# Performance work log

Measured on AMD Instinct MI355X. Metric: run time of the kernel, lower is better.

## Reference

```python
import jax, jax.numpy as jnp
import numpy as np
from jax import lax

ALIVE_THRESHOLD = 0.1
GROWTH_BOOST = 1.0  # forward default arg

_SX = jnp.array([[-1., 0., 1.], [-2., 0., 2.], [-1., 0., 1.]], dtype=jnp.float32)
_SY = jnp.array([[-1., -2., -1.], [0., 0., 0.], [1., 2., 1.]], dtype=jnp.float32)


def _depthwise3x3(x, k):
    # x: [B,C,H,W], k: [3,3] -> depthwise conv, padding 1 (SAME)
    C = x.shape[1]
    w = jnp.tile(k[None, None], (C, 1, 1, 1))  # [C,1,3,3]
    return lax.conv_general_dilated(
        x, w, window_strides=(1, 1), padding='SAME',
        dimension_numbers=('NCHW', 'OIHW', 'NCHW'), feature_group_count=C)


def _avg_pool3x3(x):
    # torch avg_pool2d(k=3, stride=1, pad=1, count_include_pad=True) == sum window / 9 with zero pad
    w = jnp.ones((1, 1, 3, 3), dtype=x.dtype) / 9.0
    return lax.conv_general_dilated(
        x, w, window_strides=(1, 1), padding='SAME',
        dimension_numbers=('NCHW', 'OIHW', 'NCHW'))


def setup_inputs() -> dict:
    key = jax.random.key(0)
    ks = jax.random.split(key, 5)
    B, C, H, W = 16, 8, 512, 512
    x = jax.random.normal(ks[0], (B, C, H, W), dtype=jnp.float32)
    # kaiming_normal_(a=0.3) -> std = sqrt(2/(1+a^2)) / sqrt(fan_in)
    gain = float(np.sqrt(2.0 / (1.0 + 0.3 ** 2)))
    w1 = jax.random.normal(ks[1], (32, 24), dtype=jnp.float32) * (gain / np.sqrt(24))
    w2 = jax.random.normal(ks[2], (32, 32), dtype=jnp.float32) * (gain / np.sqrt(32))
    w3 = jax.random.normal(ks[3], (8, 32), dtype=jnp.float32) * (gain / np.sqrt(32))
    b1 = jnp.full((32,), 0.05, dtype=jnp.float32)
    b2 = jnp.full((32,), 0.05, dtype=jnp.float32)
    b3 = jnp.full((8,), 0.05, dtype=jnp.float32)
    growth_rate = jnp.array([0.3], dtype=jnp.float32)
    return {'x': x, 'w1': w1, 'b1': b1, 'w2': w2, 'b2': b2,
            'w3': w3, 'b3': b3, 'growth_rate': growth_rate}


def reference(x, w1, b1, w2, b2, w3, b3, growth_rate):
    # perceive: [x, sobel_x(x), sobel_y(x)] -> [B, 3C, H, W]
    perceived = jnp.concatenate([x, _depthwise3x3(x, _SX), _depthwise3x3(x, _SY)], axis=1)
    # per-pixel MLP (1x1 convs)
    h = jax.nn.relu(jnp.einsum('bchw,oc->bohw', perceived, w1) + b1[None, :, None, None])
    h = jax.nn.relu(jnp.einsum('bchw,oc->bohw', h, w2) + b2[None, :, None, None])
    dx = jnp.einsum('bchw,oc->bohw', h, w3) + b3[None, :, None, None]
    dx = dx * growth_rate[0] * GROWTH_BOOST
    # alive masking / growth zones
    alive_mask = (x[:, 3:4] > ALIVE_THRESHOLD).astype(x.dtype)
    alive_ratio = jnp.mean(alive_mask)
    neighbor_alive = _avg_pool3x3(alive_mask)
    growth_zones = (neighbor_alive > 0.01).astype(x.dtype) * 0.2  # [B,1,H,W]
    boost = jnp.where(alive_ratio < 0.2, growth_zones, jnp.zeros_like(growth_zones))
    dx = jnp.concatenate([dx[:, :3], dx[:, 3:4] + boost, dx[:, 4:]], axis=1)
    new_x = jnp.clip(x + dx, -1.0, 1.0)
    alpha = jnp.clip(new_x[:, 3:4], 0.0, 1.0)
    return jnp.concatenate([new_x[:, :3], alpha, new_x[:, 4:]], axis=1)
```

## Files before the change

### kernel.cpp

```cpp
#include <hip/hip_runtime.h>

namespace {

typedef __attribute__((ext_vector_type(8))) short short8;
typedef __attribute__((ext_vector_type(4))) float f32x4;
typedef __attribute__((ext_vector_type(4))) unsigned int uint4v;

constexpr int kH = 512, kW = 512, kB = 16, kC = 8;
constexpr int kHW = kH * kW;
constexpr int kBS = kC * kHW;
constexpr int TW = 64, TH = 4;
constexpr int TWP = TW + 2, THP = TH + 2;

__global__ __launch_bounds__(256)
void alive_count_kernel(const float* __restrict__ x, int* __restrict__ cnt) {
    __shared__ int sdata[4];
    const int tid = threadIdx.x;
    const int total4 = kB * kHW / 4;
    int idx = blockIdx.x * 256 + tid;
    const int stride = gridDim.x * 256;
    int local = 0;
    const float4* x4 = (const float4*)x;
    for (int i = idx; i < total4; i += stride) {
        int b = i >> 16;
        int off = i & 65535;
        float4 v = x4[(size_t)b * (kBS / 4) + (3 * kHW / 4) + off];
        local += (v.x > 0.1f) + (v.y > 0.1f) + (v.z > 0.1f) + (v.w > 0.1f);
    }
    for (int off = 32; off > 0; off >>= 1)
        local += __shfl_down(local, off, 64);
    if ((tid & 63) == 0) sdata[tid >> 6] = local;
    __syncthreads();
    if (tid == 0) atomicAdd(cnt, sdata[0] + sdata[1] + sdata[2] + sdata[3]);
}

__device__ inline unsigned int cvt_pk_bf16(float a, float b) {
    unsigned int r;
    asm("v_cvt_pk_bf16_f32 %0, %1, %2" : "=v"(r) : "v"(a), "v"(b));
    return r;
}
__device__ inline void split_pair(float a, float b, unsigned int& h, unsigned int& l) {
    h = cvt_pk_bf16(a, b);
    float ra = a - __builtin_bit_cast(float, h << 16);
    float rb = b - __builtin_bit_cast(float, h & 0xffff0000u);
    l = cvt_pk_bf16(ra, rb);
}
__device__ inline short8 frag_of(unsigned int u0, unsigned int u1,
                                 unsigned int u2, unsigned int u3) {
    uint4v u = {u0, u1, u2, u3};
    return __builtin_bit_cast(short8, u);
}
__device__ inline void split_frag(f32x4 a, f32x4 b, short8& hi, short8& lo) {
    unsigned int h0, h1, h2, h3, l0, l1, l2, l3;
    split_pair(a.x, a.y, h0, l0);
    split_pair(a.z, a.w, h1, l1);
    split_pair(b.x, b.y, h2, l2);
    split_pair(b.z, b.w, h3, l3);
    hi = frag_of(h0, h1, h2, h3);
    lo = frag_of(l0, l1, l2, l3);
}
__device__ inline f32x4 mfma4(short8 wh, short8 wl, short8 bh, short8 bl, f32x4 acc) {
    acc = __builtin_amdgcn_mfma_f32_16x16x32_bf16(wh, bh, acc, 0, 0, 0);
    acc = __builtin_amdgcn_mfma_f32_16x16x32_bf16(wh, bl, acc, 0, 0, 0);
    acc = __builtin_amdgcn_mfma_f32_16x16x32_bf16(wl, bh, acc, 0, 0, 0);
    acc = __builtin_amdgcn_mfma_f32_16x16x32_bf16(wl, bl, acc, 0, 0, 0);
    return acc;
}
__device__ inline f32x4 relu4(f32x4 v) {
    v.x = fmaxf(v.x, 0.f); v.y = fmaxf(v.y, 0.f);
    v.z = fmaxf(v.z, 0.f); v.w = fmaxf(v.w, 0.f);
    return v;
}
__device__ inline void transpose_to_bfrag(f32x4 v0, f32x4 v1, int i1, int i2,
                                          bool oddq, bool lowq,
                                          short8& bh, short8& bl) {
    unsigned int Ah, Al, Bh, Bl, Ch, Cl, Dh, Dl;
    split_pair(v0.x, v0.y, Ah, Al);
    split_pair(v0.z, v0.w, Bh, Bl);
    split_pair(v1.x, v1.y, Ch, Cl);
    split_pair(v1.z, v1.w, Dh, Dl);
    int f1h = __builtin_amdgcn_ds_bpermute(i1, (int)(oddq ? Ch : Ah));
    int f2h = __builtin_amdgcn_ds_bpermute(i2, (int)(oddq ? Ah : Ch));
    int f3h = __builtin_amdgcn_ds_bpermute(i1, (int)(oddq ? Dh : Bh));
    int f4h = __builtin_amdgcn_ds_bpermute(i2, (int)(oddq ? Bh : Dh));
    int f1l = __builtin_amdgcn_ds_bpermute(i1, (int)(oddq ? Cl : Al));
    int f2l = __builtin_amdgcn_ds_bpermute(i2, (int)(oddq ? Al : Cl));
    int f3l = __builtin_amdgcn_ds_bpermute(i1, (int)(oddq ? Dl : Bl));
    int f4l = __builtin_amdgcn_ds_bpermute(i2, (int)(oddq ? Bl : Dl));
    bh = frag_of(lowq ? (unsigned)f1h : (unsigned)f2h, lowq ? (unsigned)f3h : (unsigned)f4h,
                 lowq ? (unsigned)f2h : (unsigned)f1h, lowq ? (unsigned)f4h : (unsigned)f3h);
    bl = frag_of(lowq ? (unsigned)f1l : (unsigned)f2l, lowq ? (unsigned)f3l : (unsigned)f4l,
                 lowq ? (unsigned)f2l : (unsigned)f1l, lowq ? (unsigned)f4l : (unsigned)f3l);
}

__global__ __launch_bounds__(256)
void nca_fused_kernel(const float* __restrict__ x,
                      const float* __restrict__ w1, const float* __restrict__ b1,
                      const float* __restrict__ w2, const float* __restrict__ b2,
                      const float* __restrict__ w3, const float* __restrict__ b3,
                      const float* __restrict__ growth,
                      const int* __restrict__ alive_cnt,
                      float* __restrict__ out) {
    __shared__ float tile[kC][THP][TWP];
    __shared__ __align__(16) unsigned int s_hi[4][64][20];
    __shared__ __align__(16) unsigned int s_lo[4][64][20];
    __shared__ __align__(16) float s_d[4][64][8];

    const int w0 = blockIdx.x * TW;
    const int h0 = blockIdx.y * TH;
    const int b  = blockIdx.z;
    const int tid = threadIdx.x;
    const int lane = tid & 63;
    const int wv = tid >> 6;
    const int m = lane & 15;
    const int q = lane >> 4;
    const bool oddq = (q & 1) != 0;
    const bool lowq = q < 2;
    const int brq = ((q & 1) << 1) | (q >> 1);
    const int i1 = (m + 16 * brq) << 2;
    const int i2 = (m + 16 * (brq ^ 1)) << 2;
    const float* xb = x + b * kBS;

    f32x4 zero4 = {0.f, 0.f, 0.f, 0.f};
    short8 w1h[2], w1l[2], w2h[2], w2l[2], w3h, w3l;
    f32x4 bias1[2], bias2[2], bias3;
#pragma unroll
    for (int mo = 0; mo < 2; ++mo) {
        int o = mo * 16 + m;
        int off = (q < 3) ? (o * 24 + q * 8) : 0;
        f32x4 wa = *(const f32x4*)(w1 + off);
        f32x4 wb = *(const f32x4*)(w1 + off + 4);
        if (q == 3) { wa = zero4; wb = zero4; }
        split_frag(wa, wb, w1h[mo], w1l[mo]);
        f32x4 wc = *(const f32x4*)(w2 + o * 32 + q * 8);
        f32x4 wd = *(const f32x4*)(w2 + o * 32 + q * 8 + 4);
        split_frag(wc, wd, w2h[mo], w2l[mo]);
        bias1[mo] = *(const f32x4*)(b1 + mo * 16 + q * 4);
        bias2[mo] = *(const f32x4*)(b2 + mo * 16 + q * 4);
    }
    {
        int off3 = (m < 8) ? (m * 32 + q * 8) : 0;
        f32x4 wa = *(const f32x4*)(w3 + off3);
        f32x4 wb = *(const f32x4*)(w3 + off3 + 4);
        if (m >= 8) { wa = zero4; wb = zero4; }
        split_frag(wa, wb, w3h, w3l);
        bias3 = zero4;
        if (lowq) bias3 = *(const f32x4*)(b3 + q * 4);
    }

    constexpr int TILE_N = kC * THP * TWP;
    for (int i = tid; i < TILE_N; i += 256) {
        int c  = i / (THP * TWP);
        int rr = i - c * (THP * TWP);
        int th = rr / TWP;
        int tw = rr - th * TWP;
        int gh = h0 + th - 1;
        int gw = w0 + tw - 1;
        float v = 0.0f;
        if ((unsigned)gh < (unsigned)kH && (unsigned)gw < (unsigned)kW)
            v = xb[c * kHW + gh * kW + gw];
        (&tile[0][0][0])[i] = v;
    }
    __syncthreads();

    const int ww = lane;
    const int hh = wv;
    float p[24];
    int nalive = 0;
#pragma unroll
    for (int c = 0; c < kC; ++c) {
        float a00 = tile[c][hh][ww],     a01 = tile[c][hh][ww + 1],     a02 = tile[c][hh][ww + 2];
        float a10 = tile[c][hh + 1][ww], a11 = tile[c][hh + 1][ww + 1], a12 = tile[c][hh + 1][ww + 2];
        float a20 = tile[c][hh + 2][ww], a21 = tile[c][hh + 2][ww + 1], a22 = tile[c][hh + 2][ww + 2];
        p[c]      = a11;
        p[8 + c]  = (a02 - a00) + 2.0f * (a12 - a10) + (a22 - a20);
        p[16 + c] = (a20 - a00) + 2.0f * (a21 - a01) + (a22 - a02);
        if (c == 3) {
            nalive = (a00 > 0.1f) + (a01 > 0.1f) + (a02 > 0.1f)
                   + (a10 > 0.1f) + (a11 > 0.1f) + (a12 > 0.1f)
                   + (a20 > 0.1f) + (a21 > 0.1f) + (a22 > 0.1f);
        }
    }
#pragma unroll
    for (int gg = 0; gg < 3; ++gg) {
        unsigned int ha, hb, hc, hd, la, lb, lc, ld;
        split_pair(p[8 * gg + 0], p[8 * gg + 1], ha, la);
        split_pair(p[8 * gg + 2], p[8 * gg + 3], hb, lb);
        split_pair(p[8 * gg + 4], p[8 * gg + 5], hc, lc);
        split_pair(p[8 * gg + 6], p[8 * gg + 7], hd, ld);
        uint4v uh = {ha, hb, hc, hd};
        uint4v ul = {la, lb, lc, ld};
        *(uint4v*)&s_hi[wv][lane][gg * 4] = uh;
        *(uint4v*)&s_lo[wv][lane][gg * 4] = ul;
    }
    {
        uint4v z = {0u, 0u, 0u, 0u};
        *(uint4v*)&s_hi[wv][lane][12] = z;
        *(uint4v*)&s_lo[wv][lane][12] = z;
    }

#pragma unroll
    for (int np = 0; np < 4; ++np) {
        const int r = np * 16 + m;
        short8 bh = __builtin_bit_cast(short8, *(const uint4v*)&s_hi[wv][r][q * 4]);
        short8 bl = __builtin_bit_cast(short8, *(const uint4v*)&s_lo[wv][r][q * 4]);
        f32x4 acc0 = bias1[0], acc1 = bias1[1];
        acc0 = mfma4(w1h[0], w1l[0], bh, bl, acc0);
        acc1 = mfma4(w1h[1], w1l[1], bh, bl, acc1);
        acc0 = relu4(acc0); acc1 = relu4(acc1);
        short8 b2fh, b2fl;
        transpose_to_bfrag(acc0, acc1, i1, i2, oddq, lowq, b2fh, b2fl);
        f32x4 acc2a = bias2[0], acc2b = bias2[1];
        acc2a = mfma4(w2h[0], w2l[0], b2fh, b2fl, acc2a);
        acc2b = mfma4(w2h[1], w2l[1], b2fh, b2fl, acc2b);
        acc2a = relu4(acc2a); acc2b = relu4(acc2b);
        short8 b3fh, b3fl;
        transpose_to_bfrag(acc2a, acc2b, i1, i2, oddq, lowq, b3fh, b3fl);
        f32x4 acc3 = bias3;
        acc3 = mfma4(w3h, w3l, b3fh, b3fl, acc3);
        if (lowq) {
            *(f32x4*)&s_d[wv][r][q * 4] = acc3;
        }
    }

    f32x4 dA = *(const f32x4*)&s_d[wv][lane][0];
    f32x4 dB = *(const f32x4*)&s_d[wv][lane][4];
    float dv[8] = {dA.x, dA.y, dA.z, dA.w, dB.x, dB.y, dB.z, dB.w};
    const float g = growth[0];
    const float ratio = (float)(*alive_cnt) * (1.0f / 4194304.0f);
    const float boost = (ratio < 0.2f && nalive > 0) ? 0.2f : 0.0f;
    float* ob = out + b * kBS + (h0 + hh) * kW + (w0 + ww);
#pragma unroll
    for (int c = 0; c < kC; ++c) {
        float v = p[c] + dv[c] * g + ((c == 3) ? boost : 0.0f);
        const float lo = (c == 3) ? 0.0f : -1.0f;
        v = fminf(fmaxf(v, lo), 1.0f);
        ob[c * kHW] = v;
    }
}

}

extern "C" void kernel_launch(void* const* d_in, const int* in_sizes, int n_in,
                              void* d_out, int out_size, void* d_ws, size_t ws_size,
                              hipStream_t stream) {
    const float* x  = (const float*)d_in[0];
    const float* w1 = (const float*)d_in[1];
    const float* b1 = (const float*)d_in[2];
    const float* w2 = (const float*)d_in[3];
    const float* b2 = (const float*)d_in[4];
    const float* w3 = (const float*)d_in[5];
    const float* b3 = (const float*)d_in[6];
    const float* gr = (const float*)d_in[7];
    float* out = (float*)d_out;
    int* cnt = (int*)d_ws;

    hipMemsetAsync(cnt, 0, sizeof(int), stream);
    alive_count_kernel<<<2048, 256, 0, stream>>>(x, cnt);
    dim3 grid(kW / TW, kH / TH, kB);
    nca_fused_kernel<<<grid, 256, 0, stream>>>(x, w1, b1, w2, b2, w3, b3, gr, cnt, out);
}
```

Before: 565.9 us.

## Permute MLP hidden-unit ordering to drop bpermute transposes and lo*lo MFMA

Weight rows are loaded in a permuted order so each layer's MFMA accumulator fragment can be reused directly as the next layer's B fragment. This removes the ds_bpermute transpose step between layers. The lo×lo bf16 MFMA term is also dropped, which cuts the MFMA count per product from four to three at a small precision cost. The packed-input staging is compacted, and the tile buffer is reused for the output staging, which needs an extra __syncthreads.

```diff
diff --git a/kernel.cpp b/kernel.cpp
--- a/kernel.cpp
+++ b/kernel.cpp
@@ -59,38 +59,16 @@
     hi = frag_of(h0, h1, h2, h3);
     lo = frag_of(l0, l1, l2, l3);
 }
-__device__ inline f32x4 mfma4(short8 wh, short8 wl, short8 bh, short8 bl, f32x4 acc) {
+__device__ inline f32x4 mfma3(short8 wh, short8 wl, short8 bh, short8 bl, f32x4 acc) {
     acc = __builtin_amdgcn_mfma_f32_16x16x32_bf16(wh, bh, acc, 0, 0, 0);
     acc = __builtin_amdgcn_mfma_f32_16x16x32_bf16(wh, bl, acc, 0, 0, 0);
     acc = __builtin_amdgcn_mfma_f32_16x16x32_bf16(wl, bh, acc, 0, 0, 0);
-    acc = __builtin_amdgcn_mfma_f32_16x16x32_bf16(wl, bl, acc, 0, 0, 0);
     return acc;
 }
 __device__ inline f32x4 relu4(f32x4 v) {
     v.x = fmaxf(v.x, 0.f); v.y = fmaxf(v.y, 0.f);
     v.z = fmaxf(v.z, 0.f); v.w = fmaxf(v.w, 0.f);
     return v;
-}
-__device__ inline void transpose_to_bfrag(f32x4 v0, f32x4 v1, int i1, int i2,
-                                          bool oddq, bool lowq,
-                                          short8& bh, short8& bl) {
-    unsigned int Ah, Al, Bh, Bl, Ch, Cl, Dh, Dl;
-    split_pair(v0.x, v0.y, Ah, Al);
-    split_pair(v0.z, v0.w, Bh, Bl);
-    split_pair(v1.x, v1.y, Ch, Cl);
-    split_pair(v1.z, v1.w, Dh, Dl);
-    int f1h = __builtin_amdgcn_ds_bpermute(i1, (int)(oddq ? Ch : Ah));
-    int f2h = __builtin_amdgcn_ds_bpermute(i2, (int)(oddq ? Ah : Ch));
-    int f3h = __builtin_amdgcn_ds_bpermute(i1, (int)(oddq ? Dh : Bh));
-    int f4h = __builtin_amdgcn_ds_bpermute(i2, (int)(oddq ? Bh : Dh));
-    int f1l = __builtin_amdgcn_ds_bpermute(i1, (int)(oddq ? Cl : Al));
-    int f2l = __builtin_amdgcn_ds_bpermute(i2, (int)(oddq ? Al : Cl));
-    int f3l = __builtin_amdgcn_ds_bpermute(i1, (int)(oddq ? Dl : Bl));
-    int f4l = __builtin_amdgcn_ds_bpermute(i2, (int)(oddq ? Bl : Dl));
-    bh = frag_of(lowq ? (unsigned)f1h : (unsigned)f2h, lowq ? (unsigned)f3h : (unsigned)f4h,
-                 lowq ? (unsigned)f2h : (unsigned)f1h, lowq ? (unsigned)f4h : (unsigned)f3h);
-    bl = frag_of(lowq ? (unsigned)f1l : (unsigned)f2l, lowq ? (unsigned)f3l : (unsigned)f4l,
-                 lowq ? (unsigned)f2l : (unsigned)f1l, lowq ? (unsigned)f4l : (unsigned)f3l);
 }
 
 __global__ __launch_bounds__(256)
@@ -101,10 +79,9 @@
                       const float* __restrict__ growth,
                       const int* __restrict__ alive_cnt,
                       float* __restrict__ out) {
-    __shared__ float tile[kC][THP][TWP];
-    __shared__ __align__(16) unsigned int s_hi[4][64][20];
-    __shared__ __align__(16) unsigned int s_lo[4][64][20];
-    __shared__ __align__(16) float s_d[4][64][8];
+    __shared__ __align__(16) float tile[kC][THP][TWP];
+    __shared__ __align__(16) unsigned int s_hi[4][64 * 12 + 4];
+    __shared__ __align__(16) unsigned int s_lo[4][64 * 12 + 4];
 
     const int w0 = blockIdx.x * TW;
     const int h0 = blockIdx.y * TH;
@@ -114,39 +91,33 @@
     const int wv = tid >> 6;
     const int m = lane & 15;
     const int q = lane >> 4;
-    const bool oddq = (q & 1) != 0;
-    const bool lowq = q < 2;
-    const int brq = ((q & 1) << 1) | (q >> 1);
-    const int i1 = (m + 16 * brq) << 2;
-    const int i2 = (m + 16 * (brq ^ 1)) << 2;
     const float* xb = x + b * kBS;
+
+    const int s0 = ((m >> 2) << 3) + (m & 3);
+    const int s1 = s0 + 4;
 
     f32x4 zero4 = {0.f, 0.f, 0.f, 0.f};
     short8 w1h[2], w1l[2], w2h[2], w2l[2], w3h, w3l;
-    f32x4 bias1[2], bias2[2], bias3;
-#pragma unroll
-    for (int mo = 0; mo < 2; ++mo) {
-        int o = mo * 16 + m;
-        int off = (q < 3) ? (o * 24 + q * 8) : 0;
-        f32x4 wa = *(const f32x4*)(w1 + off);
-        f32x4 wb = *(const f32x4*)(w1 + off + 4);
-        if (q == 3) { wa = zero4; wb = zero4; }
-        split_frag(wa, wb, w1h[mo], w1l[mo]);
-        f32x4 wc = *(const f32x4*)(w2 + o * 32 + q * 8);
-        f32x4 wd = *(const f32x4*)(w2 + o * 32 + q * 8 + 4);
-        split_frag(wc, wd, w2h[mo], w2l[mo]);
-        bias1[mo] = *(const f32x4*)(b1 + mo * 16 + q * 4);
-        bias2[mo] = *(const f32x4*)(b2 + mo * 16 + q * 4);
-    }
     {
-        int off3 = (m < 8) ? (m * 32 + q * 8) : 0;
-        f32x4 wa = *(const f32x4*)(w3 + off3);
-        f32x4 wb = *(const f32x4*)(w3 + off3 + 4);
-        if (m >= 8) { wa = zero4; wb = zero4; }
-        split_frag(wa, wb, w3h, w3l);
-        bias3 = zero4;
-        if (lowq) bias3 = *(const f32x4*)(b3 + q * 4);
-    }
+        f32x4 a = zero4, bb = zero4;
+        if (q < 3) { a = *(const f32x4*)(w1 + s0 * 24 + q * 8); bb = *(const f32x4*)(w1 + s0 * 24 + q * 8 + 4); }
+        split_frag(a, bb, w1h[0], w1l[0]);
+        a = zero4; bb = zero4;
+        if (q < 3) { a = *(const f32x4*)(w1 + s1 * 24 + q * 8); bb = *(const f32x4*)(w1 + s1 * 24 + q * 8 + 4); }
+        split_frag(a, bb, w1h[1], w1l[1]);
+        a = *(const f32x4*)(w2 + s0 * 32 + q * 8); bb = *(const f32x4*)(w2 + s0 * 32 + q * 8 + 4);
+        split_frag(a, bb, w2h[0], w2l[0]);
+        a = *(const f32x4*)(w2 + s1 * 32 + q * 8); bb = *(const f32x4*)(w2 + s1 * 32 + q * 8 + 4);
+        split_frag(a, bb, w2h[1], w2l[1]);
+        a = zero4; bb = zero4;
+        if (m < 8) { a = *(const f32x4*)(w3 + m * 32 + q * 8); bb = *(const f32x4*)(w3 + m * 32 + q * 8 + 4); }
+        split_frag(a, bb, w3h, w3l);
+    }
+    const f32x4 bias1a = *(const f32x4*)(b1 + q * 8);
+    const f32x4 bias1b = *(const f32x4*)(b1 + q * 8 + 4);
+    const f32x4 bias2a = *(const f32x4*)(b2 + q * 8);
+    const f32x4 bias2b = *(const f32x4*)(b2 + q * 8 + 4);
+    const f32x4 bias3  = (q < 2) ? *(const f32x4*)(b3 + q * 4) : zero4;
 
     constexpr int TILE_N = kC * THP * TWP;
     for (int i = tid; i < TILE_N; i += 256) {
@@ -165,66 +136,72 @@
 
     const int ww = lane;
     const int hh = wv;
-    float p[24];
+    float pc[8];
+    unsigned int hi[12], lo[12];
     int nalive = 0;
 #pragma unroll
-    for (int c = 0; c < kC; ++c) {
-        float a00 = tile[c][hh][ww],     a01 = tile[c][hh][ww + 1],     a02 = tile[c][hh][ww + 2];
-        float a10 = tile[c][hh + 1][ww], a11 = tile[c][hh + 1][ww + 1], a12 = tile[c][hh + 1][ww + 2];
-        float a20 = tile[c][hh + 2][ww], a21 = tile[c][hh + 2][ww + 1], a22 = tile[c][hh + 2][ww + 2];
-        p[c]      = a11;
-        p[8 + c]  = (a02 - a00) + 2.0f * (a12 - a10) + (a22 - a20);
-        p[16 + c] = (a20 - a00) + 2.0f * (a21 - a01) + (a22 - a02);
-        if (c == 3) {
-            nalive = (a00 > 0.1f) + (a01 > 0.1f) + (a02 > 0.1f)
-                   + (a10 > 0.1f) + (a11 > 0.1f) + (a12 > 0.1f)
-                   + (a20 > 0.1f) + (a21 > 0.1f) + (a22 > 0.1f);
+    for (int j = 0; j < 4; ++j) {
+        const int c0 = 2 * j, c1 = c0 + 1;
+        float b00 = tile[c0][hh][ww],     b01 = tile[c0][hh][ww + 1],     b02 = tile[c0][hh][ww + 2];
+        float b10 = tile[c0][hh + 1][ww], b11 = tile[c0][hh + 1][ww + 1], b12 = tile[c0][hh + 1][ww + 2];
+        float b20 = tile[c0][hh + 2][ww], b21 = tile[c0][hh + 2][ww + 1], b22 = tile[c0][hh + 2][ww + 2];
+        float c00 = tile[c1][hh][ww],     c01 = tile[c1][hh][ww + 1],     c02 = tile[c1][hh][ww + 2];
+        float c10 = tile[c1][hh + 1][ww], c11 = tile[c1][hh + 1][ww + 1], c12 = tile[c1][hh + 1][ww + 2];
+        float c20 = tile[c1][hh + 2][ww], c21 = tile[c1][hh + 2][ww + 1], c22 = tile[c1][hh + 2][ww + 2];
+        float sx0 = (b02 - b00) + 2.0f * (b12 - b10) + (b22 - b20);
+        float sy0 = (b20 - b00) + 2.0f * (b21 - b01) + (b22 - b02);
+        float sx1 = (c02 - c00) + 2.0f * (c12 - c10) + (c22 - c20);
+        float sy1 = (c20 - c00) + 2.0f * (c21 - c01) + (c22 - c02);
+        pc[c0] = b11; pc[c1] = c11;
+        if (c1 == 3) {
+            nalive = (c00 > 0.1f) + (c01 > 0.1f) + (c02 > 0.1f)
+                   + (c10 > 0.1f) + (c11 > 0.1f) + (c12 > 0.1f)
+                   + (c20 > 0.1f) + (c21 > 0.1f) + (c22 > 0.1f);
         }
-    }
-#pragma unroll
-    for (int gg = 0; gg < 3; ++gg) {
-        unsigned int ha, hb, hc, hd, la, lb, lc, ld;
-        split_pair(p[8 * gg + 0], p[8 * gg + 1], ha, la);
-        split_pair(p[8 * gg + 2], p[8 * gg + 3], hb, lb);
-        split_pair(p[8 * gg + 4], p[8 * gg + 5], hc, lc);
-        split_pair(p[8 * gg + 6], p[8 * gg + 7], hd, ld);
-        uint4v uh = {ha, hb, hc, hd};
-        uint4v ul = {la, lb, lc, ld};
-        *(uint4v*)&s_hi[wv][lane][gg * 4] = uh;
-        *(uint4v*)&s_lo[wv][lane][gg * 4] = ul;
+        split_pair(b11, c11, hi[j],     lo[j]);
+        split_pair(sx0, sx1, hi[4 + j], lo[4 + j]);
+        split_pair(sy0, sy1, hi[8 + j], lo[8 + j]);
     }
     {
-        uint4v z = {0u, 0u, 0u, 0u};
-        *(uint4v*)&s_hi[wv][lane][12] = z;
-        *(uint4v*)&s_lo[wv][lane][12] = z;
-    }
+        unsigned int* hb = &s_hi[wv][lane * 12];
+        unsigned int* lb = &s_lo[wv][lane * 12];
+        uint4v v0 = {hi[0], hi[1], hi[2], hi[3]};
+        uint4v v1 = {hi[4], hi[5], hi[6], hi[7]};
+        uint4v v2 = {hi[8], hi[9], hi[10], hi[11]};
+        *(uint4v*)hb = v0; *(uint4v*)(hb + 4) = v1; *(uint4v*)(hb + 8) = v2;
+        uint4v u0 = {lo[0], lo[1], lo[2], lo[3]};
+        uint4v u1 = {lo[4], lo[5], lo[6], lo[7]};
+        uint4v u2 = {lo[8], lo[9], lo[10], lo[11]};
+        *(uint4v*)lb = u0; *(uint4v*)(lb + 4) = u1; *(uint4v*)(lb + 8) = u2;
+    }
+    __syncthreads();
+    float* s_d = &tile[0][0][0];
 
 #pragma unroll
     for (int np = 0; np < 4; ++np) {
         const int r = np * 16 + m;
-        short8 bh = __builtin_bit_cast(short8, *(const uint4v*)&s_hi[wv][r][q * 4]);
-        short8 bl = __builtin_bit_cast(short8, *(const uint4v*)&s_lo[wv][r][q * 4]);
-        f32x4 acc0 = bias1[0], acc1 = bias1[1];
-        acc0 = mfma4(w1h[0], w1l[0], bh, bl, acc0);
-        acc1 = mfma4(w1h[1], w1l[1], bh, bl, acc1);
+        short8 bh = __builtin_bit_cast(short8, *(const uint4v*)&s_hi[wv][r * 12 + q * 4]);
+        short8 bl = __builtin_bit_cast(short8, *(const uint4v*)&s_lo[wv][r * 12 + q * 4]);
+        f32x4 acc0 = bias1a, acc1 = bias1b;
+        acc0 = mfma3(w1h[0], w1l[0], bh, bl, acc0);
+        acc1 = mfma3(w1h[1], w1l[1], bh, bl, acc1);
         acc0 = relu4(acc0); acc1 = relu4(acc1);
-        short8 b2fh, b2fl;
-        transpose_to_bfrag(acc0, acc1, i1, i2, oddq, lowq, b2fh, b2fl);
-        f32x4 acc2a = bias2[0], acc2b = bias2[1];
-        acc2a = mfma4(w2h[0], w2l[0], b2fh, b2fl, acc2a);
-        acc2b = mfma4(w2h[1], w2l[1], b2fh, b2fl, acc2b);
+        short8 b2h, b2l;
+        split_frag(acc0, acc1, b2h, b2l);
+        f32x4 acc2a = bias2a, acc2b = bias2b;
+        acc2a = mfma3(w2h[0], w2l[0], b2h, b2l, acc2a);
+        acc2b = mfma3(w2h[1], w2l[1], b2h, b2l, acc2b);
         acc2a = relu4(acc2a); acc2b = relu4(acc2b);
-        short8 b3fh, b3fl;
-        transpose_to_bfrag(acc2a, acc2b, i1, i2, oddq, lowq, b3fh, b3fl);
+        short8 b3h, b3l;
+        split_frag(acc2a, acc2b, b3h, b3l);
         f32x4 acc3 = bias3;
-        acc3 = mfma4(w3h, w3l, b3fh, b3fl, acc3);
-        if (lowq) {
-            *(f32x4*)&s_d[wv][r][q * 4] = acc3;
-        }
-    }
-
-    f32x4 dA = *(const f32x4*)&s_d[wv][lane][0];
-    f32x4 dB = *(const f32x4*)&s_d[wv][lane][4];
+        acc3 = mfma3(w3h, w3l, b3h, b3l, acc3);
+        if (q < 2)
+            *(f32x4*)&s_d[(wv * 64 + r) * 12 + q * 4] = acc3;
+    }
+
+    f32x4 dA = *(const f32x4*)&s_d[(wv * 64 + lane) * 12];
+    f32x4 dB = *(const f32x4*)&s_d[(wv * 64 + lane) * 12 + 4];
     float dv[8] = {dA.x, dA.y, dA.z, dA.w, dB.x, dB.y, dB.z, dB.w};
     const float g = growth[0];
     const float ratio = (float)(*alive_cnt) * (1.0f / 4194304.0f);
@@ -232,9 +209,9 @@
     float* ob = out + b * kBS + (h0 + hh) * kW + (w0 + ww);
 #pragma unroll
     for (int c = 0; c < kC; ++c) {
-        float v = p[c] + dv[c] * g + ((c == 3) ? boost : 0.0f);
-        const float lo = (c == 3) ? 0.0f : -1.0f;
-        v = fminf(fmaxf(v, lo), 1.0f);
+        float v = pc[c] + dv[c] * g + ((c == 3) ? boost : 0.0f);
+        const float lo2 = (c == 3) ? 0.0f : -1.0f;
+        v = fminf(fmaxf(v, lo2), 1.0f);
         ob[c * kHW] = v;
     }
 }
```

After: 473.3 us. 1.2x faster.
